# Optimization experiments

Hardware: AMD Instinct MI355X
Metric: run time of the kernel (lower is better)

The kernel has to match this reference:

```python
import jax, jax.numpy as jnp
import numpy as np

DIM = 512
CODEBOOK_SIZE = 8192
B, N = 8, 2048
EPS = 1e-12


def setup_inputs() -> dict:
    key = jax.random.key(0)
    k1, k2, k3 = jax.random.split(key, 3)
    x = jax.random.normal(k1, (B, N, DIM), dtype=jnp.float32)
    # matches torch.randn(codebook_size, dim) * dim ** -0.5
    codebook = jax.random.normal(k2, (CODEBOOK_SIZE, DIM), dtype=jnp.float32) * DIM ** -0.5
    # nn.Linear(dim, dim, bias=False) weight, applied as x @ W.T
    W = jax.random.normal(k3, (DIM, DIM), dtype=jnp.float32) * DIM ** -0.5
    return {"x": x, "codebook": codebook, "W": W}


def _l2norm(t):
    return t / jnp.maximum(jnp.linalg.norm(t, axis=-1, keepdims=True), EPS)


def _rotate_from_to(q, x):
    """Rotation trick: forward value == q, gradient flows through x via a
    detached Householder-style rotation (R = I - 2ww^T + 2 q_hat x_hat^T)
    and detached norm rescaling."""
    sg = jax.lax.stop_gradient
    norm_x = jnp.linalg.norm(x, axis=-1, keepdims=True)
    norm_q = jnp.linalg.norm(q, axis=-1, keepdims=True)
    x_hat = x / jnp.maximum(norm_x, EPS)
    q_hat = q / jnp.maximum(norm_q, EPS)
    w = sg(_l2norm(x_hat + q_hat))
    x_hat_d, q_hat_d = sg(x_hat), sg(q_hat)
    e = x
    rotated = (e
               - 2.0 * jnp.sum(e * w, axis=-1, keepdims=True) * w
               + 2.0 * jnp.sum(e * x_hat_d, axis=-1, keepdims=True) * q_hat_d)
    return rotated * sg(norm_q / jnp.maximum(norm_x, EPS))


def reference(x, codebook, W):
    # implicit codebook = Linear(codebook)
    codes = jnp.einsum('cd,ed->ce', codebook, W)  # [C, d]
    d2 = -2.0 * jnp.einsum('bnd,cd->bnc', x, codes) + jnp.sum(codes * codes, axis=-1)
    indices = jnp.argmin(jax.lax.stop_gradient(d2), axis=-1)  # [b, n] int
    quantized = codes[indices]  # gather -> [b, n, d]
    commit_loss = jnp.mean((jax.lax.stop_gradient(x) - quantized) ** 2)
    quantized = _rotate_from_to(quantized, x)
    return quantized, indices, commit_loss
```

## Files before the change

kernel.cpp:

```cpp
#include <hip/hip_runtime.h>


#define DIMK  512
#define CBN   8192
#define MROWS 16384

#define SX 24.0f
#define SC 500.0f
#define INV_SS (1.0f / (SX * SC))
#define DELTA 0.3f
#define DKEY  1231
#define NSLOT 3

#define WS_CODES   0UL
#define WS_XQ      16777216UL
#define WS_CQ      25165824UL
#define WS_NORMS   29360128UL
#define WS_CAND    29392896UL
#define WS_CBH     29392896UL
#define WS_CBL     37781504UL
#define WS_WH      54558720UL
#define WS_WL      55083008UL
#define WS_LOSSP   55607296UL

typedef short s16x8 __attribute__((ext_vector_type(8)));
typedef int   i32x4 __attribute__((ext_vector_type(4)));
typedef float f32x4 __attribute__((ext_vector_type(4)));

__device__ __forceinline__ unsigned short f2bf(float f) {
    unsigned u = __float_as_uint(f);
    unsigned r = u + 0x7FFFu + ((u >> 16) & 1u);
    return (unsigned short)(r >> 16);
}
__device__ __forceinline__ float bf2f(unsigned short h) {
    return __uint_as_float(((unsigned)h) << 16);
}
__device__ __forceinline__ void load_lds16(const void* g, void* l) {
    __builtin_amdgcn_global_load_lds((const __attribute__((address_space(1))) void*)g,
                                     (__attribute__((address_space(3))) void*)l,
                                     16, 0, 0);
}
__device__ __forceinline__ signed char q8(float v, float s) {
    return (signed char)__float2int_rn(fminf(fmaxf(v * s, -127.0f), 127.0f));
}
__device__ __forceinline__ unsigned packSlot(float d, unsigned col) {
    int k = (int)((d + 16.0f) * 4096.0f);
    k = k < 0 ? 0 : (k > 524287 ? 524287 : k);
    return ((unsigned)k << 13) | col;
}

__global__ __launch_bounds__(256) void split_bf16(const float* __restrict__ in,
                                                  unsigned short* __restrict__ hi,
                                                  unsigned short* __restrict__ lo,
                                                  int n4) {
    int i = blockIdx.x * 256 + threadIdx.x;
    if (i >= n4) return;
    float4 v = ((const float4*)in)[i];
    ushort4 h, l;
    h.x = f2bf(v.x); l.x = f2bf(v.x - bf2f(h.x));
    h.y = f2bf(v.y); l.y = f2bf(v.y - bf2f(h.y));
    h.z = f2bf(v.z); l.z = f2bf(v.z - bf2f(h.z));
    h.w = f2bf(v.w); l.w = f2bf(v.w - bf2f(h.w));
    ((ushort4*)hi)[i] = h;
    ((ushort4*)lo)[i] = l;
}

__global__ __launch_bounds__(256) void quant_x(const float* __restrict__ in,
                                               signed char* __restrict__ out, int n4) {
    int i = blockIdx.x * 256 + threadIdx.x;
    if (i >= n4) return;
    float4 v = ((const float4*)in)[i];
    char4 c;
    c.x = q8(v.x, SX); c.y = q8(v.y, SX); c.z = q8(v.z, SX); c.w = q8(v.w, SX);
    ((char4*)out)[i] = c;
}

__global__ __launch_bounds__(256) void codes_mfma(
        const unsigned short* __restrict__ Ah_g, const unsigned short* __restrict__ Al_g,
        const unsigned short* __restrict__ Bh_g, const unsigned short* __restrict__ Bl_g,
        float* __restrict__ C, signed char* __restrict__ Cq, float* __restrict__ Norms) {
    __shared__ __align__(16) unsigned short Ahi[128 * 32];
    __shared__ __align__(16) unsigned short Alo[128 * 32];
    __shared__ __align__(16) unsigned short Bhi[128 * 32];
    __shared__ __align__(16) unsigned short Blo[128 * 32];

    const int t    = threadIdx.x;
    const int w    = t >> 6;
    const int lane = t & 63;
    const int quad = lane >> 4;
    const int l16  = lane & 15;
    const int wm   = w & 1, wn = w >> 1;
    const int rowBase = blockIdx.x * 128;
    const int colBase = blockIdx.y * 128;

    f32x4 acc[4][4];
    #pragma unroll
    for (int i = 0; i < 4; ++i)
        #pragma unroll
        for (int j = 0; j < 4; ++j)
            acc[i][j] = (f32x4)(0.0f);

    const int mr = t >> 2;
    const int kq = ((t & 3) ^ ((t >> 3) & 3)) * 8;
    const size_t gxa = (size_t)(rowBase + mr) * DIMK + kq;
    const size_t gxb = gxa + (size_t)64 * DIMK;
    const size_t gca = (size_t)(colBase + mr) * DIMK + kq;
    const size_t gcb = gca + (size_t)64 * DIMK;
    const int l0 = w * 512;
    const int l1 = 2048 + w * 512;

    const int swz8 = (quad ^ ((l16 >> 1) & 3)) * 8;

    for (int k0 = 0; k0 < DIMK; k0 += 32) {
        load_lds16(Ah_g + gxa + k0, &Ahi[l0]);
        load_lds16(Ah_g + gxb + k0, &Ahi[l1]);
        load_lds16(Al_g + gxa + k0, &Alo[l0]);
        load_lds16(Al_g + gxb + k0, &Alo[l1]);
        load_lds16(Bh_g + gca + k0, &Bhi[l0]);
        load_lds16(Bh_g + gcb + k0, &Bhi[l1]);
        load_lds16(Bl_g + gca + k0, &Blo[l0]);
        load_lds16(Bl_g + gcb + k0, &Blo[l1]);
        __syncthreads();

        s16x8 ah[4], al[4], bh[4], bl[4];
        #pragma unroll
        for (int i = 0; i < 4; ++i) {
            const int m = wm * 64 + i * 16 + l16;
            ah[i] = *(const s16x8*)&Ahi[m * 32 + swz8];
            al[i] = *(const s16x8*)&Alo[m * 32 + swz8];
        }
        #pragma unroll
        for (int j = 0; j < 4; ++j) {
            const int n = wn * 64 + j * 16 + l16;
            bh[j] = *(const s16x8*)&Bhi[n * 32 + swz8];
            bl[j] = *(const s16x8*)&Blo[n * 32 + swz8];
        }
        #pragma unroll
        for (int i = 0; i < 4; ++i)
            #pragma unroll
            for (int j = 0; j < 4; ++j) {
                acc[i][j] = __builtin_amdgcn_mfma_f32_16x16x32_bf16(ah[i], bh[j], acc[i][j], 0, 0, 0);
                acc[i][j] = __builtin_amdgcn_mfma_f32_16x16x32_bf16(ah[i], bl[j], acc[i][j], 0, 0, 0);
                acc[i][j] = __builtin_amdgcn_mfma_f32_16x16x32_bf16(al[i], bh[j], acc[i][j], 0, 0, 0);
            }
        __syncthreads();
    }

    #pragma unroll
    for (int i = 0; i < 4; ++i) {
        #pragma unroll
        for (int r = 0; r < 4; ++r) {
            const int row = rowBase + wm * 64 + i * 16 + quad * 4 + r;
            float nsum = 0.0f;
            #pragma unroll
            for (int j = 0; j < 4; ++j) {
                const int col = colBase + wn * 64 + j * 16 + l16;
                const float v = acc[i][j][r];
                C[(size_t)row * DIMK + col] = v;
                Cq[(size_t)row * DIMK + col] = q8(v, SC);
                nsum = fmaf(v, v, nsum);
            }
            nsum += __shfl_xor(nsum, 1, 64);
            nsum += __shfl_xor(nsum, 2, 64);
            nsum += __shfl_xor(nsum, 4, 64);
            nsum += __shfl_xor(nsum, 8, 64);
            if (l16 == 0) atomicAdd(&Norms[row], nsum);
        }
    }
}

__global__ __launch_bounds__(256, 3) void d2_argmin_i8(
        const signed char* __restrict__ Xq,
        const signed char* __restrict__ Cq,
        const float* __restrict__ Norms,
        unsigned* __restrict__ Cand) {
    __shared__ __align__(16) signed char Ash[128 * 64];
    __shared__ __align__(16) signed char Bsh[128 * 64];

    const int t    = threadIdx.x;
    const int w    = t >> 6;
    const int lane = t & 63;
    const int quad = lane >> 4;
    const int l16  = lane & 15;
    const int wm   = w & 1, wn = w >> 1;
    const int rowBase = blockIdx.x * 128;
    const int colBase = blockIdx.y * 128;

    i32x4 acc[4][4];
    #pragma unroll
    for (int i = 0; i < 4; ++i)
        #pragma unroll
        for (int j = 0; j < 4; ++j)
            acc[i][j] = (i32x4)(0);

    const int mr  = t >> 2;
    const int kcs = ((t & 3) ^ ((t >> 3) & 3)) * 16;
    const size_t gxa = (size_t)(rowBase + mr) * DIMK + kcs;
    const size_t gxb = gxa + (size_t)64 * DIMK;
    const size_t gca = (size_t)(colBase + mr) * DIMK + kcs;
    const size_t gcb = gca + (size_t)64 * DIMK;
    const int l0 = w * 1024;
    const int l1 = 4096 + w * 1024;

    const int swz  = (quad ^ ((l16 >> 1) & 3)) * 16;
    const int aoff = (wm * 64 + l16) * 64 + swz;
    const int boff = (wn * 64 + l16) * 64 + swz;

    for (int k0 = 0; k0 < DIMK; k0 += 64) {
        load_lds16(Xq + gxa + k0, &Ash[l0]);
        load_lds16(Xq + gxb + k0, &Ash[l1]);
        load_lds16(Cq + gca + k0, &Bsh[l0]);
        load_lds16(Cq + gcb + k0, &Bsh[l1]);
        __syncthreads();

        i32x4 af[4];
        #pragma unroll
        for (int i = 0; i < 4; ++i)
            af[i] = *(const i32x4*)&Ash[aoff + i * 1024];
        #pragma unroll
        for (int j = 0; j < 4; ++j) {
            const i32x4 bfj = *(const i32x4*)&Bsh[boff + j * 1024];
            #pragma unroll
            for (int i = 0; i < 4; ++i)
                acc[i][j] = __builtin_amdgcn_mfma_i32_16x16x64_i8(af[i], bfj, acc[i][j], 0, 0, 0);
        }
        __syncthreads();
    }

    float nrm[4];
    #pragma unroll
    for (int j = 0; j < 4; ++j)
        nrm[j] = Norms[colBase + wn * 64 + j * 16 + l16];

    const int subtile = blockIdx.y * 2 + wn;
    const unsigned long long qmask = 0xFFFFull << (quad * 16);
    const unsigned long long ltm = (lane == 0) ? 0ull : (~0ull >> (64 - lane));
    const unsigned colG = colBase + wn * 64 + l16;

    #pragma unroll
    for (int i = 0; i < 4; ++i) {
        #pragma unroll
        for (int r = 0; r < 4; ++r) {
            float d0 = fmaf((float)acc[i][0][r], -2.0f * INV_SS, nrm[0]);
            float d1 = fmaf((float)acc[i][1][r], -2.0f * INV_SS, nrm[1]);
            float d2v = fmaf((float)acc[i][2][r], -2.0f * INV_SS, nrm[2]);
            float d3 = fmaf((float)acc[i][3][r], -2.0f * INV_SS, nrm[3]);
            float mn = fminf(fminf(d0, d1), fminf(d2v, d3));
            mn = fminf(mn, __shfl_xor(mn, 1, 64));
            mn = fminf(mn, __shfl_xor(mn, 2, 64));
            mn = fminf(mn, __shfl_xor(mn, 4, 64));
            mn = fminf(mn, __shfl_xor(mn, 8, 64));
            const float thr = mn + DELTA;
            unsigned long long b0 = __ballot(d0 <= thr);
            unsigned long long b1 = __ballot(d1 <= thr);
            unsigned long long b2 = __ballot(d2v <= thr);
            unsigned long long b3 = __ballot(d3 <= thr);
            const int row = rowBase + wm * 64 + i * 16 + quad * 4 + r;
            unsigned* slot = Cand + ((size_t)row * 128 + subtile) * NSLOT;
            if (d0 <= thr) {
                int rk = __popcll(b0 & qmask & ltm);
                if (rk < NSLOT) slot[rk] = packSlot(d0, colG + 0);
            }
            if (d1 <= thr) {
                int rk = __popcll(b0 & qmask) + __popcll(b1 & qmask & ltm);
                if (rk < NSLOT) slot[rk] = packSlot(d1, colG + 16);
            }
            if (d2v <= thr) {
                int rk = __popcll(b0 & qmask) + __popcll(b1 & qmask)
                       + __popcll(b2 & qmask & ltm);
                if (rk < NSLOT) slot[rk] = packSlot(d2v, colG + 32);
            }
            if (d3 <= thr) {
                int rk = __popcll(b0 & qmask) + __popcll(b1 & qmask)
                       + __popcll(b2 & qmask) + __popcll(b3 & qmask & ltm);
                if (rk < NSLOT) slot[rk] = packSlot(d3, colG + 48);
            }
        }
    }
}

__global__ __launch_bounds__(256) void refine_gather(
        const float* __restrict__ X, const float* __restrict__ Codes,
        const float* __restrict__ Norms, const unsigned* __restrict__ Cand,
        float* __restrict__ outQ, float* __restrict__ outIdx,
        float* __restrict__ lossP) {
    const int t    = threadIdx.x;
    const int w    = t >> 6;
    const int lane = t & 63;
    const int row  = blockIdx.x * 4 + w;

    const unsigned* cp = Cand + (size_t)row * 128 * NSLOT + lane * 6;
    unsigned sl[6];
    #pragma unroll
    for (int s = 0; s < 6; ++s) sl[s] = cp[s];

    unsigned mn = sl[0];
    #pragma unroll
    for (int s = 1; s < 6; ++s) mn = min(mn, sl[s]);
    #pragma unroll
    for (int mask = 1; mask < 64; mask <<= 1)
        mn = min(mn, (unsigned)__shfl((int)mn, lane ^ mask, 64));
    const unsigned thrp = (((mn >> 13) + DKEY) << 13) | 0x1FFFu;

    const float4 xa = *(const float4*)(X + (size_t)row * DIMK + lane * 8);
    const float4 xb = *(const float4*)(X + (size_t)row * DIMK + lane * 8 + 4);

    float bestD = __builtin_inff();
    unsigned bestIdx = 0xFFFFFFFFu;

    #pragma unroll
    for (int s = 0; s < 6; ++s) {
        unsigned long long bm = __ballot(sl[s] <= thrp);
        while (bm) {
            const int src = __ffsll(bm) - 1;
            bm &= bm - 1;
            const unsigned sv = (unsigned)__shfl((int)sl[s], src, 64);
            const unsigned idx = sv & 0x1FFFu;
            const float4 ca = *(const float4*)(Codes + (size_t)idx * DIMK + lane * 8);
            const float4 cbv = *(const float4*)(Codes + (size_t)idx * DIMK + lane * 8 + 4);
            float s2 = xa.x * ca.x + xa.y * ca.y + xa.z * ca.z + xa.w * ca.w
                     + xb.x * cbv.x + xb.y * cbv.y + xb.z * cbv.z + xb.w * cbv.w;
            #pragma unroll
            for (int mm = 1; mm < 64; mm <<= 1) s2 += __shfl_xor(s2, mm, 64);
            const float d2 = fmaf(-2.0f, s2, Norms[idx]);
            if (d2 < bestD || (d2 == bestD && idx < bestIdx)) { bestD = d2; bestIdx = idx; }
        }
    }

    const float4 qa = *(const float4*)(Codes + (size_t)bestIdx * DIMK + lane * 8);
    const float4 qb = *(const float4*)(Codes + (size_t)bestIdx * DIMK + lane * 8 + 4);
    *(float4*)(outQ + (size_t)row * DIMK + lane * 8) = qa;
    *(float4*)(outQ + (size_t)row * DIMK + lane * 8 + 4) = qb;
    float dx0 = xa.x - qa.x, dx1 = xa.y - qa.y, dx2 = xa.z - qa.z, dx3 = xa.w - qa.w;
    float dy0 = xb.x - qb.x, dy1 = xb.y - qb.y, dy2 = xb.z - qb.z, dy3 = xb.w - qb.w;
    float s = dx0 * dx0 + dx1 * dx1 + dx2 * dx2 + dx3 * dx3
            + dy0 * dy0 + dy1 * dy1 + dy2 * dy2 + dy3 * dy3;
    #pragma unroll
    for (int off = 32; off > 0; off >>= 1) s += __shfl_down(s, off);
    if (lane == 0) {
        lossP[row] = s;
        outIdx[row] = (float)bestIdx;
    }
}

__global__ __launch_bounds__(256) void finalize_loss(const float* __restrict__ lossPartials,
                                                     float* __restrict__ outLoss) {
    const int t = threadIdx.x;
    float s = 0.0f;
    for (int i = t; i < MROWS; i += 256) s += lossPartials[i];
    #pragma unroll
    for (int off = 32; off > 0; off >>= 1) s += __shfl_down(s, off);
    __shared__ float red[4];
    if ((t & 63) == 0) red[t >> 6] = s;
    __syncthreads();
    if (t == 0)
        *outLoss = (red[0] + red[1] + red[2] + red[3]) * (1.0f / (float)((size_t)MROWS * DIMK));
}

extern "C" void kernel_launch(void* const* d_in, const int* in_sizes, int n_in,
                              void* d_out, int out_size, void* d_ws, size_t ws_size,
                              hipStream_t stream) {
    const float* x  = (const float*)d_in[0];
    const float* cb = (const float*)d_in[1];
    const float* W  = (const float*)d_in[2];
    float* out = (float*)d_out;

    char* ws = (char*)d_ws;
    float* codes          = (float*)(ws + WS_CODES);
    signed char* xq       = (signed char*)(ws + WS_XQ);
    signed char* cq       = (signed char*)(ws + WS_CQ);
    float* norms          = (float*)(ws + WS_NORMS);
    unsigned* cand        = (unsigned*)(ws + WS_CAND);
    unsigned short* cbh   = (unsigned short*)(ws + WS_CBH);
    unsigned short* cbl   = (unsigned short*)(ws + WS_CBL);
    unsigned short* wh    = (unsigned short*)(ws + WS_WH);
    unsigned short* wl    = (unsigned short*)(ws + WS_WL);
    float* lossP          = (float*)(ws + WS_LOSSP);

    hipMemsetAsync(norms, 0, CBN * 4, stream);

    split_bf16<<<(CBN * DIMK / 4 + 255) / 256, 256, 0, stream>>>(cb, cbh, cbl, CBN * DIMK / 4);
    split_bf16<<<(DIMK * DIMK / 4 + 255) / 256, 256, 0, stream>>>(W, wh, wl, DIMK * DIMK / 4);
    quant_x<<<(MROWS * DIMK / 4 + 255) / 256, 256, 0, stream>>>(x, xq, MROWS * DIMK / 4);

    codes_mfma<<<dim3(CBN / 128, DIMK / 128), 256, 0, stream>>>(cbh, cbl, wh, wl, codes, cq, norms);

    hipMemsetAsync(cand, 0xFF, (size_t)MROWS * 128 * NSLOT * 4, stream);

    d2_argmin_i8<<<dim3(MROWS / 128, CBN / 128), 256, 0, stream>>>(xq, cq, norms, cand);

    refine_gather<<<MROWS / 4, 256, 0, stream>>>(x, codes, norms, cand, out,
                                                 out + (size_t)MROWS * DIMK, lossP);
    finalize_loss<<<1, 256, 0, stream>>>(lossP, out + (size_t)MROWS * DIMK + MROWS);
}
```

Before: 315.4 us.

## Fuse prep kernels, use 8-wave d2 tiles, and keep top-3 via sorting network

Merges the two bf16-split kernels, the x quantization and the norms memset into one prep launch. The d2_argmin kernel now runs 512 threads with each wave covering 32 rows, which halves accumulator registers per wave and raises the occupancy target. The threshold/ballot candidate selection is replaced by a packed-key top-3 per row found with min/max shuffles, so every slot is written and the 0xFF memset of the candidate buffer can be dropped. In exchange, the candidate set changes from a distance-threshold rule to an exact top-3, and each wave does more shuffle work in the epilogue.

Result: faster. 292.5 us (-7.3%).

```diff
diff --git a/kernel.cpp b/kernel.cpp
--- a/kernel.cpp
+++ b/kernel.cpp
@@ -8,7 +8,6 @@
 #define SX 24.0f
 #define SC 500.0f
 #define INV_SS (1.0f / (SX * SC))
-#define DELTA 0.3f
 #define DKEY  1231
 #define NSLOT 3
 
@@ -43,36 +42,45 @@
 __device__ __forceinline__ signed char q8(float v, float s) {
     return (signed char)__float2int_rn(fminf(fmaxf(v * s, -127.0f), 127.0f));
 }
-__device__ __forceinline__ unsigned packSlot(float d, unsigned col) {
-    int k = (int)((d + 16.0f) * 4096.0f);
-    k = k < 0 ? 0 : (k > 524287 ? 524287 : k);
-    return ((unsigned)k << 13) | col;
-}
-
-__global__ __launch_bounds__(256) void split_bf16(const float* __restrict__ in,
-                                                  unsigned short* __restrict__ hi,
-                                                  unsigned short* __restrict__ lo,
-                                                  int n4) {
-    int i = blockIdx.x * 256 + threadIdx.x;
-    if (i >= n4) return;
-    float4 v = ((const float4*)in)[i];
-    ushort4 h, l;
-    h.x = f2bf(v.x); l.x = f2bf(v.x - bf2f(h.x));
-    h.y = f2bf(v.y); l.y = f2bf(v.y - bf2f(h.y));
-    h.z = f2bf(v.z); l.z = f2bf(v.z - bf2f(h.z));
-    h.w = f2bf(v.w); l.w = f2bf(v.w - bf2f(h.w));
-    ((ushort4*)hi)[i] = h;
-    ((ushort4*)lo)[i] = l;
-}
-
-__global__ __launch_bounds__(256) void quant_x(const float* __restrict__ in,
-                                               signed char* __restrict__ out, int n4) {
-    int i = blockIdx.x * 256 + threadIdx.x;
-    if (i >= n4) return;
-    float4 v = ((const float4*)in)[i];
-    char4 c;
-    c.x = q8(v.x, SX); c.y = q8(v.y, SX); c.z = q8(v.z, SX); c.w = q8(v.w, SX);
-    ((char4*)out)[i] = c;
+
+__global__ __launch_bounds__(256) void prep(
+        const float* __restrict__ x, const float* __restrict__ cb, const float* __restrict__ W,
+        signed char* __restrict__ xq,
+        unsigned short* __restrict__ cbh, unsigned short* __restrict__ cbl,
+        unsigned short* __restrict__ wh, unsigned short* __restrict__ wl,
+        float* __restrict__ norms) {
+    const int b = blockIdx.x;
+    const int t = threadIdx.x;
+    if (b < 8192) {
+        const int i = b * 256 + t;
+        float4 v = ((const float4*)x)[i];
+        char4 c;
+        c.x = q8(v.x, SX); c.y = q8(v.y, SX); c.z = q8(v.z, SX); c.w = q8(v.w, SX);
+        ((char4*)xq)[i] = c;
+    } else if (b < 12288) {
+        const int i = (b - 8192) * 256 + t;
+        float4 v = ((const float4*)cb)[i];
+        ushort4 h, l;
+        h.x = f2bf(v.x); l.x = f2bf(v.x - bf2f(h.x));
+        h.y = f2bf(v.y); l.y = f2bf(v.y - bf2f(h.y));
+        h.z = f2bf(v.z); l.z = f2bf(v.z - bf2f(h.z));
+        h.w = f2bf(v.w); l.w = f2bf(v.w - bf2f(h.w));
+        ((ushort4*)cbh)[i] = h;
+        ((ushort4*)cbl)[i] = l;
+    } else if (b < 12544) {
+        const int i = (b - 12288) * 256 + t;
+        float4 v = ((const float4*)W)[i];
+        ushort4 h, l;
+        h.x = f2bf(v.x); l.x = f2bf(v.x - bf2f(h.x));
+        h.y = f2bf(v.y); l.y = f2bf(v.y - bf2f(h.y));
+        h.z = f2bf(v.z); l.z = f2bf(v.z - bf2f(h.z));
+        h.w = f2bf(v.w); l.w = f2bf(v.w - bf2f(h.w));
+        ((ushort4*)wh)[i] = h;
+        ((ushort4*)wl)[i] = l;
+    } else {
+        const int i = (b - 12544) * 256 + t;
+        norms[i] = 0.0f;
+    }
 }
 
 __global__ __launch_bounds__(256) void codes_mfma(
@@ -169,7 +177,7 @@
     }
 }
 
-__global__ __launch_bounds__(256, 3) void d2_argmin_i8(
+__global__ __launch_bounds__(512, 6) void d2_argmin_i8(
         const signed char* __restrict__ Xq,
         const signed char* __restrict__ Cq,
         const float* __restrict__ Norms,
@@ -182,13 +190,13 @@
     const int lane = t & 63;
     const int quad = lane >> 4;
     const int l16  = lane & 15;
-    const int wm   = w & 1, wn = w >> 1;
+    const int wm   = w & 3, wn = w >> 2;
     const int rowBase = blockIdx.x * 128;
     const int colBase = blockIdx.y * 128;
 
-    i32x4 acc[4][4];
-    #pragma unroll
-    for (int i = 0; i < 4; ++i)
+    i32x4 acc[2][4];
+    #pragma unroll
+    for (int i = 0; i < 2; ++i)
         #pragma unroll
         for (int j = 0; j < 4; ++j)
             acc[i][j] = (i32x4)(0);
@@ -196,84 +204,75 @@
     const int mr  = t >> 2;
     const int kcs = ((t & 3) ^ ((t >> 3) & 3)) * 16;
     const size_t gxa = (size_t)(rowBase + mr) * DIMK + kcs;
-    const size_t gxb = gxa + (size_t)64 * DIMK;
     const size_t gca = (size_t)(colBase + mr) * DIMK + kcs;
-    const size_t gcb = gca + (size_t)64 * DIMK;
-    const int l0 = w * 1024;
-    const int l1 = 4096 + w * 1024;
+    const int lb = w * 1024;
 
     const int swz  = (quad ^ ((l16 >> 1) & 3)) * 16;
-    const int aoff = (wm * 64 + l16) * 64 + swz;
+    const int aoff = (wm * 32 + l16) * 64 + swz;
     const int boff = (wn * 64 + l16) * 64 + swz;
 
+    float nq[4];
+    #pragma unroll
+    for (int j = 0; j < 4; ++j)
+        nq[j] = fmaf(Norms[colBase + wn * 64 + j * 16 + l16], 4096.0f, 65536.0f);
+
     for (int k0 = 0; k0 < DIMK; k0 += 64) {
-        load_lds16(Xq + gxa + k0, &Ash[l0]);
-        load_lds16(Xq + gxb + k0, &Ash[l1]);
-        load_lds16(Cq + gca + k0, &Bsh[l0]);
-        load_lds16(Cq + gcb + k0, &Bsh[l1]);
+        load_lds16(Xq + gxa + k0, &Ash[lb]);
+        load_lds16(Cq + gca + k0, &Bsh[lb]);
         __syncthreads();
 
-        i32x4 af[4];
-        #pragma unroll
-        for (int i = 0; i < 4; ++i)
-            af[i] = *(const i32x4*)&Ash[aoff + i * 1024];
+        i32x4 af[2];
+        af[0] = *(const i32x4*)&Ash[aoff];
+        af[1] = *(const i32x4*)&Ash[aoff + 1024];
         #pragma unroll
         for (int j = 0; j < 4; ++j) {
             const i32x4 bfj = *(const i32x4*)&Bsh[boff + j * 1024];
-            #pragma unroll
-            for (int i = 0; i < 4; ++i)
-                acc[i][j] = __builtin_amdgcn_mfma_i32_16x16x64_i8(af[i], bfj, acc[i][j], 0, 0, 0);
+            acc[0][j] = __builtin_amdgcn_mfma_i32_16x16x64_i8(af[0], bfj, acc[0][j], 0, 0, 0);
+            acc[1][j] = __builtin_amdgcn_mfma_i32_16x16x64_i8(af[1], bfj, acc[1][j], 0, 0, 0);
         }
         __syncthreads();
     }
 
-    float nrm[4];
-    #pragma unroll
-    for (int j = 0; j < 4; ++j)
-        nrm[j] = Norms[colBase + wn * 64 + j * 16 + l16];
-
+    const unsigned colG = colBase + wn * 64 + l16;
     const int subtile = blockIdx.y * 2 + wn;
-    const unsigned long long qmask = 0xFFFFull << (quad * 16);
-    const unsigned long long ltm = (lane == 0) ? 0ull : (~0ull >> (64 - lane));
-    const unsigned colG = colBase + wn * 64 + l16;
-
-    #pragma unroll
-    for (int i = 0; i < 4; ++i) {
+    const float C2 = -8192.0f * INV_SS;
+
+    #pragma unroll
+    for (int i = 0; i < 2; ++i) {
         #pragma unroll
         for (int r = 0; r < 4; ++r) {
-            float d0 = fmaf((float)acc[i][0][r], -2.0f * INV_SS, nrm[0]);
-            float d1 = fmaf((float)acc[i][1][r], -2.0f * INV_SS, nrm[1]);
-            float d2v = fmaf((float)acc[i][2][r], -2.0f * INV_SS, nrm[2]);
-            float d3 = fmaf((float)acc[i][3][r], -2.0f * INV_SS, nrm[3]);
-            float mn = fminf(fminf(d0, d1), fminf(d2v, d3));
-            mn = fminf(mn, __shfl_xor(mn, 1, 64));
-            mn = fminf(mn, __shfl_xor(mn, 2, 64));
-            mn = fminf(mn, __shfl_xor(mn, 4, 64));
-            mn = fminf(mn, __shfl_xor(mn, 8, 64));
-            const float thr = mn + DELTA;
-            unsigned long long b0 = __ballot(d0 <= thr);
-            unsigned long long b1 = __ballot(d1 <= thr);
-            unsigned long long b2 = __ballot(d2v <= thr);
-            unsigned long long b3 = __ballot(d3 <= thr);
-            const int row = rowBase + wm * 64 + i * 16 + quad * 4 + r;
-            unsigned* slot = Cand + ((size_t)row * 128 + subtile) * NSLOT;
-            if (d0 <= thr) {
-                int rk = __popcll(b0 & qmask & ltm);
-                if (rk < NSLOT) slot[rk] = packSlot(d0, colG + 0);
-            }
-            if (d1 <= thr) {
-                int rk = __popcll(b0 & qmask) + __popcll(b1 & qmask & ltm);
-                if (rk < NSLOT) slot[rk] = packSlot(d1, colG + 16);
-            }
-            if (d2v <= thr) {
-                int rk = __popcll(b0 & qmask) + __popcll(b1 & qmask)
-                       + __popcll(b2 & qmask & ltm);
-                if (rk < NSLOT) slot[rk] = packSlot(d2v, colG + 32);
-            }
-            if (d3 <= thr) {
-                int rk = __popcll(b0 & qmask) + __popcll(b1 & qmask)
-                       + __popcll(b2 & qmask) + __popcll(b3 & qmask & ltm);
-                if (rk < NSLOT) slot[rk] = packSlot(d3, colG + 48);
+            unsigned k[4];
+            #pragma unroll
+            for (int j = 0; j < 4; ++j) {
+                const float kf = fmaf((float)acc[i][j][r], C2, nq[j]);
+                int ki = (int)kf;
+                ki = ki < 0 ? 0 : ki;
+                ki = ki > 524287 ? 524287 : ki;
+                k[j] = ((unsigned)ki << 13) | (colG + j * 16);
+            }
+            unsigned lo01 = min(k[0], k[1]), hi01 = max(k[0], k[1]);
+            unsigned lo23 = min(k[2], k[3]), hi23 = max(k[2], k[3]);
+            unsigned a0 = min(lo01, lo23);
+            unsigned m  = max(lo01, lo23);
+            unsigned tt = min(hi01, hi23);
+            unsigned a1 = min(m, tt);
+            unsigned a2 = max(m, tt);
+            #pragma unroll
+            for (int mk = 1; mk < 16; mk <<= 1) {
+                const unsigned b0 = __shfl_xor(a0, mk, 64);
+                const unsigned b1 = __shfl_xor(a1, mk, 64);
+                const unsigned b2 = __shfl_xor(a2, mk, 64);
+                const unsigned M0 = max(a0, b0);
+                const unsigned m1 = min(a1, b1);
+                const unsigned n0 = min(a0, b0);
+                a2 = min(max(m1, M0), min(a2, b2));
+                a1 = min(M0, m1);
+                a0 = n0;
+            }
+            if (l16 == 0) {
+                const int row = rowBase + wm * 32 + i * 16 + quad * 4 + r;
+                unsigned* slot = Cand + ((size_t)row * 128 + subtile) * NSLOT;
+                slot[0] = a0; slot[1] = a1; slot[2] = a2;
             }
         }
     }
@@ -377,17 +376,11 @@
     unsigned short* wl    = (unsigned short*)(ws + WS_WL);
     float* lossP          = (float*)(ws + WS_LOSSP);
 
-    hipMemsetAsync(norms, 0, CBN * 4, stream);
-
-    split_bf16<<<(CBN * DIMK / 4 + 255) / 256, 256, 0, stream>>>(cb, cbh, cbl, CBN * DIMK / 4);
-    split_bf16<<<(DIMK * DIMK / 4 + 255) / 256, 256, 0, stream>>>(W, wh, wl, DIMK * DIMK / 4);
-    quant_x<<<(MROWS * DIMK / 4 + 255) / 256, 256, 0, stream>>>(x, xq, MROWS * DIMK / 4);
+    prep<<<12576, 256, 0, stream>>>(x, cb, W, xq, cbh, cbl, wh, wl, norms);
 
     codes_mfma<<<dim3(CBN / 128, DIMK / 128), 256, 0, stream>>>(cbh, cbl, wh, wl, codes, cq, norms);
 
-    hipMemsetAsync(cand, 0xFF, (size_t)MROWS * 128 * NSLOT * 4, stream);
-
-    d2_argmin_i8<<<dim3(MROWS / 128, CBN / 128), 256, 0, stream>>>(xq, cq, norms, cand);
+    d2_argmin_i8<<<dim3(MROWS / 128, CBN / 128), 512, 0, stream>>>(xq, cq, norms, cand);
 
     refine_gather<<<MROWS / 4, 256, 0, stream>>>(x, codes, norms, cand, out,
                                                  out + (size_t)MROWS * DIMK, lossP);
```
